# Kernel optimization log

Measured on AMD Instinct MI355X. Metric: run time of the kernel, lower is better.

The kernel has to match this reference:

```python
import jax, jax.numpy as jnp
import numpy as np

HIDDEN_DIM = 1024
NUM_HEADS = 16
HEAD_DIM = HIDDEN_DIM // NUM_HEADS
SCALAR_NORM = float(np.sqrt(HIDDEN_DIM / NUM_HEADS))


def setup_inputs() -> dict:
    key = jax.random.key(0)
    k1, k2 = jax.random.split(key)
    B, N, D = 2, 2048, HIDDEN_DIM
    x = jax.random.normal(k1, (B, N, D), dtype=jnp.float32)
    # torch Linear weight shape: (3D, D); xavier_uniform-like scale
    limit = float(np.sqrt(6.0 / (D + 3 * D)))
    W_qkv = jax.random.uniform(k2, (3 * D, D), dtype=jnp.float32, minval=-limit, maxval=limit)
    return {"x": x, "W_qkv": W_qkv}


def reference(x, W_qkv):
    b, n, d = x.shape
    h, hd = NUM_HEADS, HEAD_DIM
    qkv = x @ W_qkv.T  # (B, N, 3D)
    q, k, v = jnp.split(qkv, 3, axis=-1)
    # (B, H, N, hd)
    q = q.reshape(b, n, h, hd).transpose(0, 2, 1, 3)
    k = k.reshape(b, n, h, hd).transpose(0, 2, 1, 3)
    v = v.reshape(b, n, h, hd).transpose(0, 2, 1, 3)
    scores = jnp.einsum('bhik,bhjk->bhij', q, k) / SCALAR_NORM
    attn = jax.nn.softmax(scores, axis=-1)
    out = jnp.einsum('bhij,bhjk->bhik', attn, v)
    return out.transpose(0, 2, 1, 3).reshape(b, n, d)
```

## Files before the change

### kernel.cpp

```cpp
#include <hip/hip_runtime.h>
#include <hip/hip_bf16.h>

#define SEQ 2048
#define DMODEL 1024
#define NHEADS 16
#define HD 64
#define BATCH 2

typedef short bf16x8 __attribute__((ext_vector_type(8)));
typedef float f32x4 __attribute__((ext_vector_type(4)));
typedef float f32x16 __attribute__((ext_vector_type(16)));

static __device__ inline ushort f2bf(float f) {
    unsigned u = __float_as_uint(f);
    return (ushort)((u + 0x7fffu + ((u >> 16) & 1u)) >> 16);
}

static __device__ inline unsigned pk2bf(float a, float b) {
    __hip_bfloat162 h = __float22bfloat162_rn(make_float2(a, b));
    union { __hip_bfloat162 h; unsigned u; } c; c.h = h;
    return c.u;
}

static __device__ inline void async16(const ushort* g, ushort* l) {
    __builtin_amdgcn_global_load_lds((const __attribute__((address_space(1))) void*)g,
                                     (__attribute__((address_space(3))) void*)l, 16, 0, 0);
}

static __device__ inline void plane32swap(unsigned& a, unsigned& b) {
    asm volatile("v_permlane32_swap_b32 %0, %1" : "+v"(a), "+v"(b));
}

union GemmSmem {
    struct { ushort A[128 * 64]; ushort B[128 * 64]; } st;
    ushort C[128 * 128];
};

__global__ __launch_bounds__(256) void qkv_gemm(
        const float* __restrict__ Xf, const float* __restrict__ Wf,
        ushort* __restrict__ Qd, ushort* __restrict__ Kd, ushort* __restrict__ Vd) {
    __shared__ GemmSmem sm;
    const int t = threadIdx.x;
    const int lane = t & 63, l15 = lane & 15, quad = lane >> 4;
    const int w = t >> 6, wm = w >> 1, wn = w & 1;
    const int gm = blockIdx.x, gn = blockIdx.y;
    const int srow = t >> 3, scol = (t & 7) * 8;

    const float* pX = &Xf[(gm * 128 + srow) * 1024 + scol];
    const float* pW = &Wf[(gn * 128 + srow) * 1024 + scol];

    f32x4 acc[4][4] = {};

    for (int kt = 0; kt < 16; ++kt) {
        const int k0 = kt * 64;
        __syncthreads();
        float4 ra[8], rb[8];
#pragma unroll
        for (int inst = 0; inst < 4; ++inst) {
            const float* a = pX + inst * 32 * 1024 + k0;
            const float* b = pW + inst * 32 * 1024 + k0;
            ra[inst * 2]     = *(const float4*)a;
            ra[inst * 2 + 1] = *(const float4*)(a + 4);
            rb[inst * 2]     = *(const float4*)b;
            rb[inst * 2 + 1] = *(const float4*)(b + 4);
        }
#pragma unroll
        for (int inst = 0; inst < 4; ++inst) {
            union { unsigned u[4]; bf16x8 v; } ua, ub;
            ua.u[0] = pk2bf(ra[inst * 2].x,     ra[inst * 2].y);
            ua.u[1] = pk2bf(ra[inst * 2].z,     ra[inst * 2].w);
            ua.u[2] = pk2bf(ra[inst * 2 + 1].x, ra[inst * 2 + 1].y);
            ua.u[3] = pk2bf(ra[inst * 2 + 1].z, ra[inst * 2 + 1].w);
            *(bf16x8*)&sm.st.A[inst * 2048 + t * 8] = ua.v;
            ub.u[0] = pk2bf(rb[inst * 2].x,     rb[inst * 2].y);
            ub.u[1] = pk2bf(rb[inst * 2].z,     rb[inst * 2].w);
            ub.u[2] = pk2bf(rb[inst * 2 + 1].x, rb[inst * 2 + 1].y);
            ub.u[3] = pk2bf(rb[inst * 2 + 1].z, rb[inst * 2 + 1].w);
            *(bf16x8*)&sm.st.B[inst * 2048 + t * 8] = ub.v;
        }
        __syncthreads();
#pragma unroll
        for (int ks = 0; ks < 2; ++ks) {
            const int kk = ks * 32 + quad * 8;
            bf16x8 af[4], bfr[4];
#pragma unroll
            for (int i = 0; i < 4; ++i) {
                af[i]  = *(const bf16x8*)&sm.st.A[(wm * 64 + i * 16 + l15) * 64 + kk];
                bfr[i] = *(const bf16x8*)&sm.st.B[(wn * 64 + i * 16 + l15) * 64 + kk];
            }
#pragma unroll
            for (int i = 0; i < 4; ++i)
#pragma unroll
                for (int j = 0; j < 4; ++j)
                    acc[i][j] = __builtin_amdgcn_mfma_f32_16x16x32_bf16(af[i], bfr[j], acc[i][j], 0, 0, 0);
        }
    }

    __syncthreads();
    if (gn < 16) {
        const float sc = (gn < 8) ? (0.125f * 1.44269504f) : 1.0f;
#pragma unroll
        for (int i = 0; i < 4; ++i)
#pragma unroll
            for (int reg = 0; reg < 4; ++reg) {
                const int row = wm * 64 + i * 16 + quad * 4 + reg;
                const int sw = (row & 7) * 8;
#pragma unroll
                for (int jp = 0; jp < 4; jp += 2) {
                    unsigned u = pk2bf(acc[i][jp][reg] * sc, acc[i][jp + 1][reg] * sc);
                    sm.C[row * 128 + ((wn * 64 + jp * 16 + l15) ^ sw)] = (ushort)u;
                    sm.C[row * 128 + ((wn * 64 + (jp + 1) * 16 + l15) ^ sw)] = (ushort)(u >> 16);
                }
            }
        __syncthreads();

        ushort* dst = (gn < 8) ? Qd : Kd;
        const int rloc = t >> 4, l = t & 15;
#pragma unroll
        for (int pass = 0; pass < 8; ++pass) {
            const int r = pass * 16 + rloc;
            bf16x8 v = *(const bf16x8*)&sm.C[r * 128 + ((l * 8) ^ ((r & 7) * 8))];
            const int ng = gm * 128 + r;
            const int b = ng >> 11, n = ng & 2047;
            const int cl = (gn * 128 + l * 8) & 1023;
            const int h = cl >> 6, hd = cl & 63;
            *(bf16x8*)&dst[(((b * NHEADS + h) * SEQ) + n) * HD + hd] = v;
        }
    } else {
#pragma unroll
        for (int i = 0; i < 4; ++i)
#pragma unroll
            for (int reg = 0; reg < 4; ++reg) {
                const int nloc = wm * 64 + i * 16 + quad * 4 + reg;
#pragma unroll
                for (int jp = 0; jp < 4; ++jp) {
                    const int f = wn * 64 + jp * 16 + l15;
                    sm.C[f * 128 + (nloc ^ ((f & 7) * 8))] = f2bf(acc[i][jp][reg]);
                }
            }
        __syncthreads();

        const int rloc = t >> 4, l = t & 15;
        const int b = gm >> 4;
        const int n0 = (gm & 15) * 128 + l * 8;
#pragma unroll
        for (int pass = 0; pass < 8; ++pass) {
            const int r = pass * 16 + rloc;
            bf16x8 v = *(const bf16x8*)&sm.C[r * 128 + ((l * 8) ^ ((r & 7) * 8))];
            const int cl = (gn * 128 + r) & 1023;
            const int h = cl >> 6, hd = cl & 63;
            *(bf16x8*)&Vd[(((long)(b * NHEADS + h) * HD) + hd) * SEQ + n0] = v;
        }
    }
}

__global__ __launch_bounds__(256, 1) void attn_kernel(
        const ushort* __restrict__ Q, const ushort* __restrict__ K,
        const ushort* __restrict__ VT, float* __restrict__ O) {
    __shared__ ushort sK[2][128 * 64];
    __shared__ ushort sVT[2][64 * 128];
    __shared__ float sL[4][64];

    const int t = threadIdx.x;
    const int lane = t & 63, l31 = lane & 31, hi = lane >> 5;
    const int w = t >> 6;

    const int flat = blockIdx.y * gridDim.x + blockIdx.x;
    const int qt = (flat >> 3) & 7;
    const int bh = (flat & 7) + ((flat >> 6) << 3);

    const ushort* Qp = Q + ((long)bh * SEQ + qt * 256 + w * 64) * HD;
    const ushort* Kp = K + (long)bh * SEQ * HD;
    const ushort* Vp = VT + (long)bh * HD * SEQ;

    bf16x8 bq[2][4];
#pragma unroll
    for (int qh = 0; qh < 2; ++qh)
#pragma unroll
        for (int ks = 0; ks < 4; ++ks)
            bq[qh][ks] = *(const bf16x8*)&Qp[(qh * 32 + l31) * HD + ks * 16 + hi * 8];

    const int krow = t >> 3;
    const int kcol = ((t & 7) ^ (krow & 7)) * 8;
    const ushort* gK = Kp + krow * HD + kcol;
    const int vrow = t >> 4;
    const int vcol = ((t & 15) ^ (vrow & 7)) * 8;
    const ushort* gV = Vp + (long)vrow * SEQ + vcol;

    ushort* lK[2] = { &sK[0][t * 8], &sK[1][t * 8] };
    ushort* lV[2] = { &sVT[0][t * 8], &sVT[1][t * 8] };

    f32x16 accA[2] = {}, accB[2] = {};
    f32x4 LpA = {}, LpB = {};
    const int swz = (l31 & 7) << 3;

#pragma unroll
    for (int c = 0; c < 4; ++c) {
        async16(gK + c * 32 * HD, lK[0] + c * 2048);
        async16(gV + (long)c * 16 * SEQ, lV[0] + c * 2048);
    }
    __syncthreads();

    for (int kt = 0; kt < 16; ++kt) {
        const int cur = kt & 1;
        if (kt < 15) {
            const ushort* nK = gK + (kt + 1) * 128 * HD;
            const ushort* nV = gV + (kt + 1) * 128;
#pragma unroll
            for (int c = 0; c < 4; ++c) {
                async16(nK + c * 32 * HD, lK[cur ^ 1] + c * 2048);
                async16(nV + (long)c * 16 * SEQ, lV[cur ^ 1] + c * 2048);
            }
        }
        const ushort* bK = sK[cur];
        const ushort* bV = sVT[cur];

        f32x16 sA[4], sB[4];
#pragma unroll
        for (int nb = 0; nb < 4; ++nb) {
            f32x16 zA = {}, zB = {};
#pragma unroll
            for (int ks = 0; ks < 4; ++ks) {
                bf16x8 ak = *(const bf16x8*)&bK[(nb * 32 + l31) * 64 + ((ks * 16 + hi * 8) ^ swz)];
                zA = __builtin_amdgcn_mfma_f32_32x32x16_bf16(ak, bq[0][ks], zA, 0, 0, 0);
                zB = __builtin_amdgcn_mfma_f32_32x32x16_bf16(ak, bq[1][ks], zB, 0, 0, 0);
            }
            sA[nb] = zA; sB[nb] = zB;
        }

#pragma unroll
        for (int h = 0; h < 2; ++h) {
            bf16x8 paA[4], paB[4];
#pragma unroll
            for (int nb2 = 0; nb2 < 2; ++nb2) {
                float pA[16], pB[16];
#pragma unroll
                for (int r = 0; r < 16; ++r) {
                    pA[r] = __builtin_amdgcn_exp2f(sA[h * 2 + nb2][r]);
                    pB[r] = __builtin_amdgcn_exp2f(sB[h * 2 + nb2][r]);
                }
#pragma unroll
                for (int r = 0; r < 16; ++r) { LpA[r & 3] += pA[r]; LpB[r & 3] += pB[r]; }
#pragma unroll
                for (int h2 = 0; h2 < 2; ++h2) {
                    const int b = 8 * h2;
                    unsigned a0 = pk2bf(pA[b + 0], pA[b + 1]);
                    unsigned a1 = pk2bf(pA[b + 2], pA[b + 3]);
                    unsigned a2 = pk2bf(pA[b + 4], pA[b + 5]);
                    unsigned a3 = pk2bf(pA[b + 6], pA[b + 7]);
                    plane32swap(a0, a2);
                    plane32swap(a1, a3);
                    union { unsigned u[4]; bf16x8 v; } fa;
                    fa.u[0] = a0; fa.u[1] = a1; fa.u[2] = a2; fa.u[3] = a3;
                    paA[nb2 * 2 + h2] = fa.v;
                    unsigned b0 = pk2bf(pB[b + 0], pB[b + 1]);
                    unsigned b1 = pk2bf(pB[b + 2], pB[b + 3]);
                    unsigned b2 = pk2bf(pB[b + 4], pB[b + 5]);
                    unsigned b3 = pk2bf(pB[b + 6], pB[b + 7]);
                    plane32swap(b0, b2);
                    plane32swap(b1, b3);
                    union { unsigned u[4]; bf16x8 v; } fb;
                    fb.u[0] = b0; fb.u[1] = b1; fb.u[2] = b2; fb.u[3] = b3;
                    paB[nb2 * 2 + h2] = fb.v;
                }
            }
#pragma unroll
            for (int db = 0; db < 2; ++db)
#pragma unroll
                for (int ks = 0; ks < 4; ++ks) {
                    bf16x8 vf = *(const bf16x8*)&bV[(db * 32 + l31) * 128 + h * 64 + ((ks * 16 + hi * 8) ^ swz)];
                    accA[db] = __builtin_amdgcn_mfma_f32_32x32x16_bf16(paA[ks], vf, accA[db], 0, 0, 0);
                    accB[db] = __builtin_amdgcn_mfma_f32_32x32x16_bf16(paB[ks], vf, accB[db], 0, 0, 0);
                }
        }

        __syncthreads();
    }

    {
        const float la = (LpA[0] + LpA[1]) + (LpA[2] + LpA[3]);
        unsigned lu = __float_as_uint(la), lv = lu;
        plane32swap(lu, lv);
        const float lb = (LpB[0] + LpB[1]) + (LpB[2] + LpB[3]);
        unsigned mu = __float_as_uint(lb), mv = mu;
        plane32swap(mu, mv);
        if (hi == 0) {
            sL[w][l31]      = __uint_as_float(lu) + __uint_as_float(lv);
            sL[w][32 + l31] = __uint_as_float(mu) + __uint_as_float(mv);
        }
    }
    __syncthreads();

    const int b = bh >> 4, h = bh & 15;
    const int qg0 = qt * 256 + w * 64;
#pragma unroll
    for (int r = 0; r < 16; ++r) {
        const int ql = (r & 3) + 8 * (r >> 2) + 4 * hi;
        const float invA = 1.0f / sL[w][ql];
        const float invB = 1.0f / sL[w][32 + ql];
#pragma unroll
        for (int db = 0; db < 2; ++db) {
            O[((long)b * SEQ + qg0 + ql) * DMODEL + h * HD + db * 32 + l31]      = accA[db][r] * invA;
            O[((long)b * SEQ + qg0 + 32 + ql) * DMODEL + h * HD + db * 32 + l31] = accB[db][r] * invB;
        }
    }
}

extern "C" void kernel_launch(void* const* d_in, const int* in_sizes, int n_in,
                              void* d_out, int out_size, void* d_ws, size_t ws_size,
                              hipStream_t stream) {
    const float* x  = (const float*)d_in[0];
    const float* Wq = (const float*)d_in[1];
    float* out = (float*)d_out;

    const int NQKV = BATCH * NHEADS * SEQ * HD;

    ushort* q  = (ushort*)d_ws;
    ushort* k  = q + NQKV;
    ushort* vt = k + NQKV;

    dim3 g1(4096 / 128, 3072 / 128);
    qkv_gemm<<<g1, 256, 0, stream>>>(x, Wq, q, k, vt);

    dim3 g2(SEQ / 256, BATCH * NHEADS);
    attn_kernel<<<g2, 256, 0, stream>>>(q, k, vt, out);
}
```

Baseline: 189.1 us.

## Double-buffer QKV GEMM shared tiles, swizzle LDS layout, remap block order

The QKV projection GEMM now double-buffers its LDS tiles and prefetches global loads two k-steps ahead in registers, so global latency overlaps the MFMA work and only one barrier is needed per k-step. The LDS A/B layout is XOR-swizzled by row to avoid bank conflicts on the fragment reads. The block index is also remapped so consecutive workgroups spread across M/N tiles, aiming for better L2 reuse. The cost is extra registers for the prefetched float4s and twice the staging LDS (the union already sized C to match).

Result: faster. 175.1 us (-7.4%).

```diff
diff --git a/kernel.cpp b/kernel.cpp
--- a/kernel.cpp
+++ b/kernel.cpp
@@ -32,7 +32,7 @@
 }
 
 union GemmSmem {
-    struct { ushort A[128 * 64]; ushort B[128 * 64]; } st;
+    struct { ushort A[128 * 64]; ushort B[128 * 64]; } st[2];
     ushort C[128 * 128];
 };
 
@@ -43,56 +43,82 @@
     const int t = threadIdx.x;
     const int lane = t & 63, l15 = lane & 15, quad = lane >> 4;
     const int w = t >> 6, wm = w >> 1, wn = w & 1;
-    const int gm = blockIdx.x, gn = blockIdx.y;
-    const int srow = t >> 3, scol = (t & 7) * 8;
-
-    const float* pX = &Xf[(gm * 128 + srow) * 1024 + scol];
-    const float* pW = &Wf[(gn * 128 + srow) * 1024 + scol];
+
+    const int f0 = blockIdx.y * gridDim.x + blockIdx.x;
+    const int nf = (f0 & 7) * 96 + (f0 >> 3);
+    const int gm = nf / 24, gn = nf % 24;
+
+    const int srow = t >> 3;
+    const int sg = t & 7;
+    const int wslot = sg ^ (srow & 7);
+    const float* pX = &Xf[(gm * 128 + srow) * 1024 + sg * 8];
+    const float* pW = &Wf[(gn * 128 + srow) * 1024 + sg * 8];
 
     f32x4 acc[4][4] = {};
+    float4 ra[8], rb[8];
+
+    auto gload = [&](int kt) {
+#pragma unroll
+        for (int i = 0; i < 4; ++i) {
+            const float* a = pX + i * 32 * 1024 + kt * 64;
+            const float* b = pW + i * 32 * 1024 + kt * 64;
+            ra[i * 2]     = *(const float4*)a;
+            ra[i * 2 + 1] = *(const float4*)(a + 4);
+            rb[i * 2]     = *(const float4*)b;
+            rb[i * 2 + 1] = *(const float4*)(b + 4);
+        }
+    };
+    auto swrite = [&](int buf) {
+        ushort* A = sm.st[buf].A;
+        ushort* B = sm.st[buf].B;
+#pragma unroll
+        for (int i = 0; i < 4; ++i) {
+            union { unsigned u[4]; bf16x8 v; } ua, ub;
+            ua.u[0] = pk2bf(ra[i * 2].x,     ra[i * 2].y);
+            ua.u[1] = pk2bf(ra[i * 2].z,     ra[i * 2].w);
+            ua.u[2] = pk2bf(ra[i * 2 + 1].x, ra[i * 2 + 1].y);
+            ua.u[3] = pk2bf(ra[i * 2 + 1].z, ra[i * 2 + 1].w);
+            *(bf16x8*)&A[(i * 32 + srow) * 64 + wslot * 8] = ua.v;
+            ub.u[0] = pk2bf(rb[i * 2].x,     rb[i * 2].y);
+            ub.u[1] = pk2bf(rb[i * 2].z,     rb[i * 2].w);
+            ub.u[2] = pk2bf(rb[i * 2 + 1].x, rb[i * 2 + 1].y);
+            ub.u[3] = pk2bf(rb[i * 2 + 1].z, rb[i * 2 + 1].w);
+            *(bf16x8*)&B[(i * 32 + srow) * 64 + wslot * 8] = ub.v;
+        }
+    };
+
+    gload(0);
+    swrite(0);
+    gload(1);
+    asm volatile("s_waitcnt lgkmcnt(0)" ::: "memory");
+    __builtin_amdgcn_s_barrier();
+    __builtin_amdgcn_sched_barrier(0);
 
     for (int kt = 0; kt < 16; ++kt) {
-        const int k0 = kt * 64;
-        __syncthreads();
-        float4 ra[8], rb[8];
-#pragma unroll
-        for (int inst = 0; inst < 4; ++inst) {
-            const float* a = pX + inst * 32 * 1024 + k0;
-            const float* b = pW + inst * 32 * 1024 + k0;
-            ra[inst * 2]     = *(const float4*)a;
-            ra[inst * 2 + 1] = *(const float4*)(a + 4);
-            rb[inst * 2]     = *(const float4*)b;
-            rb[inst * 2 + 1] = *(const float4*)(b + 4);
-        }
-#pragma unroll
-        for (int inst = 0; inst < 4; ++inst) {
-            union { unsigned u[4]; bf16x8 v; } ua, ub;
-            ua.u[0] = pk2bf(ra[inst * 2].x,     ra[inst * 2].y);
-            ua.u[1] = pk2bf(ra[inst * 2].z,     ra[inst * 2].w);
-            ua.u[2] = pk2bf(ra[inst * 2 + 1].x, ra[inst * 2 + 1].y);
-            ua.u[3] = pk2bf(ra[inst * 2 + 1].z, ra[inst * 2 + 1].w);
-            *(bf16x8*)&sm.st.A[inst * 2048 + t * 8] = ua.v;
-            ub.u[0] = pk2bf(rb[inst * 2].x,     rb[inst * 2].y);
-            ub.u[1] = pk2bf(rb[inst * 2].z,     rb[inst * 2].w);
-            ub.u[2] = pk2bf(rb[inst * 2 + 1].x, rb[inst * 2 + 1].y);
-            ub.u[3] = pk2bf(rb[inst * 2 + 1].z, rb[inst * 2 + 1].w);
-            *(bf16x8*)&sm.st.B[inst * 2048 + t * 8] = ub.v;
-        }
-        __syncthreads();
+        const int buf = kt & 1;
+        const ushort* A = sm.st[buf].A;
+        const ushort* B = sm.st[buf].B;
 #pragma unroll
         for (int ks = 0; ks < 2; ++ks) {
-            const int kk = ks * 32 + quad * 8;
+            const int off = ((ks * 4 + quad) ^ (l15 & 7)) * 8;
             bf16x8 af[4], bfr[4];
 #pragma unroll
             for (int i = 0; i < 4; ++i) {
-                af[i]  = *(const bf16x8*)&sm.st.A[(wm * 64 + i * 16 + l15) * 64 + kk];
-                bfr[i] = *(const bf16x8*)&sm.st.B[(wn * 64 + i * 16 + l15) * 64 + kk];
+                af[i]  = *(const bf16x8*)&A[(wm * 64 + i * 16 + l15) * 64 + off];
+                bfr[i] = *(const bf16x8*)&B[(wn * 64 + i * 16 + l15) * 64 + off];
             }
 #pragma unroll
             for (int i = 0; i < 4; ++i)
 #pragma unroll
                 for (int j = 0; j < 4; ++j)
                     acc[i][j] = __builtin_amdgcn_mfma_f32_16x16x32_bf16(af[i], bfr[j], acc[i][j], 0, 0, 0);
+        }
+        if (kt < 15) {
+            swrite(buf ^ 1);
+            if (kt < 14) gload(kt + 2);
+            asm volatile("s_waitcnt lgkmcnt(0)" ::: "memory");
+            __builtin_amdgcn_s_barrier();
+            __builtin_amdgcn_sched_barrier(0);
         }
     }
 
```
